# Performance work log

Measured on AMD Instinct MI355X. Metric: run time of the kernel, lower is better.

## Reference

```python
import jax, jax.numpy as jnp
import numpy as np

B, T, D = 16, 2048, 768


def sinusoidal_pe(t, d, dtype):
    # standard transformer sinusoidal positional encoding [t, d]
    pos = jnp.arange(t, dtype=jnp.float32)[:, None]            # [t,1]
    i = jnp.arange(d // 2, dtype=jnp.float32)[None, :]          # [1,d/2]
    ang = pos / jnp.power(10000.0, 2.0 * i / d)                 # [t,d/2]
    pe = jnp.concatenate([jnp.sin(ang), jnp.cos(ang)], axis=-1) # [t,d]
    return pe.astype(dtype)


def setup_inputs() -> dict:
    key = jax.random.key(0)
    k1, k2, k3 = jax.random.split(key, 3)
    wav_features = jax.random.normal(k1, (B, T, D), dtype=jnp.float32)
    # right-aligned padding: per-sample valid lengths in [T//2, T]
    lens = jax.random.randint(k2, (B,), T // 2, T + 1)
    feature_padding_mask = jnp.arange(T)[None, :] >= lens[:, None]       # [B,T] bool
    # patchout mask: Bernoulli(0.5) over frames (the masker)
    non_visible_mask = jax.random.bernoulli(k3, 0.5, (B, T))             # [B,T] bool
    return {
        "wav_features": wav_features,
        "non_visible_mask": non_visible_mask,
        "feature_padding_mask": feature_padding_mask,
    }


def reference(wav_features, non_visible_mask, feature_padding_mask):
    # training-path mask(): add PE, then per-row compact the visible,
    # non-padded frames to the front (ragged gather), zero-pad the rest.
    b, t, d = wav_features.shape
    to_mask = wav_features + sinusoidal_pe(t, d, wav_features.dtype)[None]  # [B,T,D]
    keep = jnp.logical_and(~non_visible_mask, ~feature_padding_mask)        # [B,T]
    # stable argsort on ~keep puts kept indices first, in original order ==
    # prefix-sum-offset gather (torch boolean-index semantics)
    order = jnp.argsort(~keep, axis=1, stable=True)                         # [B,T]
    visible = jnp.take_along_axis(to_mask, order[:, :, None], axis=1)       # [B,T,D]
    visible_lens = keep.sum(axis=1)                                          # [B]
    visible_padding_mask = jnp.arange(t)[None, :] >= visible_lens[:, None]  # [B,T]
    # torch pads ragged rows with zeros; we pad to static T (>= maxlen) for jit
    visible = jnp.where(visible_padding_mask[:, :, None],
                        jnp.zeros((), visible.dtype), visible)
    return visible, visible_padding_mask, visible_lens
```

## Files before the change

kernel.cpp:

```cpp
#include <hip/hip_runtime.h>

#define BB 16
#define TT 2048
#define DD 768

__global__ void pm_scan_kernel(const int* __restrict__ nonvis,
                               const int* __restrict__ pad,
                               int* __restrict__ src_idx,
                               int* __restrict__ lens,
                               float* __restrict__ out_mask,
                               float* __restrict__ out_lens) {
    const int b = blockIdx.x;
    const int tid = threadIdx.x;
    const int base_t = tid * 8;

    const int* nv = nonvis + b * TT;
    const int* pd = pad + b * TT;

    int keep[8];
    int cnt = 0;
#pragma unroll
    for (int k = 0; k < 8; ++k) {
        const int t = base_t + k;
        const int kp = (nv[t] == 0) && (pd[t] == 0);
        keep[k] = kp;
        cnt += kp;
    }

    __shared__ int sdata[256];
    sdata[tid] = cnt;
    __syncthreads();

    for (int off = 1; off < 256; off <<= 1) {
        int v = 0;
        if (tid >= off) v = sdata[tid - off];
        __syncthreads();
        sdata[tid] += v;
        __syncthreads();
    }

    const int incl = sdata[tid];
    const int total = sdata[255];
    int pos = incl - cnt;

    int* si = src_idx + b * TT;
#pragma unroll
    for (int k = 0; k < 8; ++k) {
        if (keep[k]) {
            si[pos] = base_t + k;
            ++pos;
        }
    }

    float* om = out_mask + b * TT;
#pragma unroll
    for (int k = 0; k < 8; ++k) {
        const int t = base_t + k;
        om[t] = (t >= total) ? 1.0f : 0.0f;
    }

    if (tid == 0) {
        lens[b] = total;
        out_lens[b] = (float)total;
    }
}

__global__ void pm_gather_kernel(const float* __restrict__ wav,
                                 const int* __restrict__ src_idx,
                                 const int* __restrict__ lens,
                                 float* __restrict__ out) {
    const int gid = blockIdx.x * blockDim.x + threadIdx.x;
    const int D4 = DD / 4;
    const int d4 = gid % D4;
    const int row = gid / D4;
    const int j = row & (TT - 1);
    const int b = row >> 11;

    float4 v = make_float4(0.f, 0.f, 0.f, 0.f);
    if (j < lens[b]) {
        const int t = src_idx[b * TT + j];
        const float4 a =
            reinterpret_cast<const float4*>(wav + ((size_t)(b * TT + t)) * DD)[d4];
        const int d0 = d4 * 4;
        const float tf = (float)t;
        float pe[4];
#pragma unroll
        for (int k = 0; k < 4; ++k) {
            const int d = d0 + k;
            const int i = (d < DD / 2) ? d : (d - DD / 2);
            const float inv = __expf(-0.0239852613853510f * (float)i);
            const float ang = tf * inv;
            pe[k] = (d < DD / 2) ? __sinf(ang) : __cosf(ang);
        }
        v = make_float4(a.x + pe[0], a.y + pe[1], a.z + pe[2], a.w + pe[3]);
    }
    reinterpret_cast<float4*>(out)[gid] = v;
}

extern "C" void kernel_launch(void* const* d_in, const int* in_sizes, int n_in,
                              void* d_out, int out_size, void* d_ws, size_t ws_size,
                              hipStream_t stream) {
    const float* wav   = (const float*)d_in[0];
    const int* nonvis  = (const int*)d_in[1];
    const int* pad     = (const int*)d_in[2];

    float* out       = (float*)d_out;
    float* out_vis   = out;
    float* out_mask  = out + (size_t)BB * TT * DD;
    float* out_lens  = out_mask + BB * TT;

    int* src_idx = (int*)d_ws;
    int* lens    = src_idx + BB * TT;

    pm_scan_kernel<<<BB, 256, 0, stream>>>(nonvis, pad, src_idx, lens,
                                           out_mask, out_lens);

    const int n4 = BB * TT * DD / 4;
    pm_gather_kernel<<<n4 / 256, 256, 0, stream>>>(wav, src_idx, lens, out_vis);
}
```

Measured before the change: 29.78 us.

## Use wave shuffle scan, vectorized mask IO, and nontemporal output stores

The scan kernel now loads masks as int4, does a 64-lane shuffle-up scan plus a small cross-wave combine instead of a 256-entry shared-memory scan with many barriers, and writes the output mask as float4. The gather kernel writes its output with nontemporal stores so the large streaming write bypasses cache retention. The scan kernel is tiny and runs once per batch, so most of any effect would come from the nontemporal stores on the ~100MB output.

Result: faster. 28.65 us (-3.8%).

```diff
diff --git a/kernel.cpp b/kernel.cpp
--- a/kernel.cpp
+++ b/kernel.cpp
@@ -3,6 +3,8 @@
 #define BB 16
 #define TT 2048
 #define DD 768
+
+typedef float f32x4 __attribute__((ext_vector_type(4)));
 
 __global__ void pm_scan_kernel(const int* __restrict__ nonvis,
                                const int* __restrict__ pad,
@@ -13,34 +15,47 @@
     const int b = blockIdx.x;
     const int tid = threadIdx.x;
     const int base_t = tid * 8;
+    const int lane = tid & 63;
+    const int wid = tid >> 6;
 
-    const int* nv = nonvis + b * TT;
-    const int* pd = pad + b * TT;
+    const int4* nv4 = reinterpret_cast<const int4*>(nonvis + b * TT) + tid * 2;
+    const int4* pd4 = reinterpret_cast<const int4*>(pad + b * TT) + tid * 2;
+    const int4 nva = nv4[0], nvb = nv4[1];
+    const int4 pda = pd4[0], pdb = pd4[1];
 
     int keep[8];
+    keep[0] = (nva.x == 0) && (pda.x == 0);
+    keep[1] = (nva.y == 0) && (pda.y == 0);
+    keep[2] = (nva.z == 0) && (pda.z == 0);
+    keep[3] = (nva.w == 0) && (pda.w == 0);
+    keep[4] = (nvb.x == 0) && (pdb.x == 0);
+    keep[5] = (nvb.y == 0) && (pdb.y == 0);
+    keep[6] = (nvb.z == 0) && (pdb.z == 0);
+    keep[7] = (nvb.w == 0) && (pdb.w == 0);
+
     int cnt = 0;
 #pragma unroll
-    for (int k = 0; k < 8; ++k) {
-        const int t = base_t + k;
-        const int kp = (nv[t] == 0) && (pd[t] == 0);
-        keep[k] = kp;
-        cnt += kp;
+    for (int k = 0; k < 8; ++k) cnt += keep[k];
+
+    int x = cnt;
+#pragma unroll
+    for (int off = 1; off < 64; off <<= 1) {
+        const int v = __shfl_up(x, off);
+        if (lane >= off) x += v;
     }
 
-    __shared__ int sdata[256];
-    sdata[tid] = cnt;
+    __shared__ int wtot[4];
+    if (lane == 63) wtot[wid] = x;
     __syncthreads();
 
-    for (int off = 1; off < 256; off <<= 1) {
-        int v = 0;
-        if (tid >= off) v = sdata[tid - off];
-        __syncthreads();
-        sdata[tid] += v;
-        __syncthreads();
-    }
+    const int t0 = wtot[0], t1 = wtot[1], t2 = wtot[2], t3 = wtot[3];
+    const int total = t0 + t1 + t2 + t3;
+    int wbase = 0;
+    if (wid > 0) wbase += t0;
+    if (wid > 1) wbase += t1;
+    if (wid > 2) wbase += t2;
 
-    const int incl = sdata[tid];
-    const int total = sdata[255];
+    const int incl = wbase + x;
     int pos = incl - cnt;
 
     int* si = src_idx + b * TT;
@@ -52,12 +67,12 @@
         }
     }
 
-    float* om = out_mask + b * TT;
+    float m[8];
 #pragma unroll
-    for (int k = 0; k < 8; ++k) {
-        const int t = base_t + k;
-        om[t] = (t >= total) ? 1.0f : 0.0f;
-    }
+    for (int k = 0; k < 8; ++k) m[k] = (base_t + k >= total) ? 1.0f : 0.0f;
+    float4* om4 = reinterpret_cast<float4*>(out_mask + b * TT) + tid * 2;
+    om4[0] = make_float4(m[0], m[1], m[2], m[3]);
+    om4[1] = make_float4(m[4], m[5], m[6], m[7]);
 
     if (tid == 0) {
         lens[b] = total;
@@ -76,11 +91,11 @@
     const int j = row & (TT - 1);
     const int b = row >> 11;
 
-    float4 v = make_float4(0.f, 0.f, 0.f, 0.f);
+    f32x4 v = (f32x4)(0.f, 0.f, 0.f, 0.f);
     if (j < lens[b]) {
         const int t = src_idx[b * TT + j];
-        const float4 a =
-            reinterpret_cast<const float4*>(wav + ((size_t)(b * TT + t)) * DD)[d4];
+        const f32x4 a =
+            reinterpret_cast<const f32x4*>(wav + ((size_t)(b * TT + t)) * DD)[d4];
         const int d0 = d4 * 4;
         const float tf = (float)t;
         float pe[4];
@@ -92,9 +107,9 @@
             const float ang = tf * inv;
             pe[k] = (d < DD / 2) ? __sinf(ang) : __cosf(ang);
         }
-        v = make_float4(a.x + pe[0], a.y + pe[1], a.z + pe[2], a.w + pe[3]);
+        v = (f32x4)(a.x + pe[0], a.y + pe[1], a.z + pe[2], a.w + pe[3]);
     }
-    reinterpret_cast<float4*>(out)[gid] = v;
+    __builtin_nontemporal_store(v, reinterpret_cast<f32x4*>(out) + gid);
 }
 
 extern "C" void kernel_launch(void* const* d_in, const int* in_sizes, int n_in,
```
